# Kernel optimization log

Hardware: AMD Instinct MI355X
Metric: run time of the kernel (lower is better)

Reference implementation:

```python
import jax, jax.numpy as jnp
import numpy as np

D_MODEL = 1024
H = 16
D_K = D_MODEL // H


def setup_inputs() -> dict:
    key = jax.random.key(0)
    ks = jax.random.split(key, 11)
    B, S = 4, 2048
    scale = 1.0 / np.sqrt(D_MODEL)
    inp = {
        "q": jax.random.normal(ks[0], (B, S, D_MODEL), jnp.float32),
        "k": jax.random.normal(ks[1], (B, S, D_MODEL), jnp.float32),
        "v": jax.random.normal(ks[2], (B, S, D_MODEL), jnp.float32),
        # Linear weights stored as (in, out) so y = x @ W + b
        "W_q": jax.random.normal(ks[3], (D_MODEL, D_MODEL), jnp.float32) * scale,
        "b_q": jnp.zeros((D_MODEL,), jnp.float32),
        "W_k": jax.random.normal(ks[4], (D_MODEL, D_MODEL), jnp.float32) * scale,
        "b_k": jnp.zeros((D_MODEL,), jnp.float32),
        "W_v": jax.random.normal(ks[5], (D_MODEL, D_MODEL), jnp.float32) * scale,
        "b_v": jnp.zeros((D_MODEL,), jnp.float32),
        "W_o": jax.random.normal(ks[6], (D_MODEL, D_MODEL), jnp.float32) * scale,
        "b_o": jnp.zeros((D_MODEL,), jnp.float32),
    }
    return inp


def _split_heads(x, B):
    # (B, S, d_model) -> (B, h, S, d_k)
    return x.reshape(B, -1, H, D_K).transpose(0, 2, 1, 3)


def reference(q, k, v, W_q, b_q, W_k, b_k, W_v, b_v, W_o, b_o):
    B = q.shape[0]
    qh = _split_heads(q @ W_q + b_q, B)  # (B,h,S,dk)
    kh = _split_heads(k @ W_k + b_k, B)
    vh = _split_heads(v @ W_v + b_v, B)
    scores = jnp.einsum("bhsd,bhtd->bhst", qh, kh) / jnp.sqrt(jnp.float32(D_K))
    attn = jax.nn.softmax(scores, axis=-1)  # dropout p=0 -> identity
    out = jnp.einsum("bhst,bhtd->bhsd", attn, vh)  # (B,h,S,dk)
    out = out.transpose(0, 2, 1, 3).reshape(B, -1, H * D_K)  # merge heads
    return out @ W_o + b_o
```

## Files before the change

### kernel.cpp

```cpp
#include <hip/hip_runtime.h>

#define D_MODEL 1024
#define SEQ 2048
#define BATCH 4
#define NHEADS 16
#define HDK 64
#define MTOT (BATCH * SEQ)
#define NT (SEQ / 64)

typedef __attribute__((ext_vector_type(8))) _Float16 f16x8;
typedef __attribute__((ext_vector_type(2))) __fp16 pk16x2;
typedef __attribute__((ext_vector_type(4))) float f32x4;

__device__ inline unsigned short f2h_bits(float f) {
  _Float16 h = (_Float16)f;
  union { _Float16 h; unsigned short u; } c;
  c.h = h;
  return c.u;
}

__device__ inline unsigned pk2(float a, float b) {
  union { pk16x2 h; unsigned u; } c;
  c.h = __builtin_amdgcn_cvt_pkrtz(a, b);
  return c.u;
}

typedef __attribute__((address_space(3))) unsigned int lds_u32_t;
typedef __attribute__((address_space(1))) const unsigned int glb_u32_t;
__device__ __forceinline__ void gll16(const void* g, void* l) {
  __builtin_amdgcn_global_load_lds((glb_u32_t*)g, (lds_u32_t*)l, 16, 0, 0);
}

__global__ __launch_bounds__(256) void wtrans_kernel(
    const float* __restrict__ W0, const float* __restrict__ W1,
    const float* __restrict__ W2, const float* __restrict__ W3,
    unsigned short* __restrict__ WT) {
  __shared__ float tile[64][65];
  const float* W = blockIdx.z == 0 ? W0 : blockIdx.z == 1 ? W1
                  : blockIdx.z == 2 ? W2 : W3;
  unsigned short* out = WT + (size_t)blockIdx.z * D_MODEL * D_MODEL;
  const int k0 = blockIdx.x * 64, n0 = blockIdx.y * 64;
  const int t = threadIdx.x;
#pragma unroll
  for (int i = 0; i < 16; ++i) {
    int e = t + i * 256;
    int r = e >> 6, c = e & 63;
    tile[r][c] = W[(size_t)(k0 + r) * D_MODEL + n0 + c];
  }
  __syncthreads();
#pragma unroll
  for (int i = 0; i < 16; ++i) {
    int e = t + i * 256;
    int r = e >> 6, c = e & 63;
    int slot = (c >> 3) ^ (r & 7);
    out[(size_t)(n0 + r) * D_MODEL + k0 + slot * 8 + (c & 7)] =
        f2h_bits(tile[c][r]);
  }
}

template <bool A_F32, int OUT_MODE>
__global__ __launch_bounds__(256) void gemm_kernel(
    const void* __restrict__ Aptr, const unsigned short* __restrict__ Bt,
    const float* __restrict__ bias, void* __restrict__ Cptr) {
  __shared__ unsigned short As[128 * 64];
  __shared__ unsigned short Bs[128 * 64];
  const int t = threadIdx.x;
  const int lane = t & 63, w = t >> 6;
  const int lo16 = lane & 15, g = lane >> 4;
  const int wr = w >> 1, wc = w & 1;
  const int m0 = blockIdx.x * 128, n0 = blockIdx.y * 128;

  f32x4 acc[4][4] = {};

  const unsigned short* bgb =
      Bt + (size_t)(n0 + (t >> 3)) * D_MODEL + (t & 7) * 8;
  const float* agf = nullptr;
  const unsigned short* agh = nullptr;
  if constexpr (A_F32)
    agf = (const float*)Aptr + (size_t)(m0 + (t >> 4)) * D_MODEL + (t & 15) * 4;
  else
    agh = (const unsigned short*)Aptr + (size_t)(m0 + (t >> 3)) * D_MODEL +
          (t & 7) * 8;

  for (int kt = 0; kt < D_MODEL / 64; ++kt) {
#pragma unroll
    for (int i = 0; i < 4; ++i)
      gll16(bgb + (size_t)i * 32 * D_MODEL, &Bs[(size_t)(i * 256 + t) * 8]);
    bgb += 64;

    if constexpr (A_F32) {
#pragma unroll
      for (int i = 0; i < 8; ++i) {
        int row = (t >> 4) + i * 16, kq = (t & 15) * 4;
        float4 vv =
            *reinterpret_cast<const float4*>(agf + (size_t)i * 16 * D_MODEL);
        int slot = (kq >> 3) ^ (row & 7);
        uint2 pp;
        pp.x = pk2(vv.x, vv.y);
        pp.y = pk2(vv.z, vv.w);
        *reinterpret_cast<uint2*>(&As[row * 64 + slot * 8 + (kq & 7)]) = pp;
      }
      agf += 64;
    } else {
#pragma unroll
      for (int i = 0; i < 4; ++i)
        gll16(agh + (size_t)i * 32 * D_MODEL, &As[(size_t)(i * 256 + t) * 8]);
      agh += 64;
    }
    __syncthreads();

#pragma unroll
    for (int kk = 0; kk < 2; ++kk) {
      f16x8 af[4], bfr[4];
#pragma unroll
      for (int m = 0; m < 4; ++m) {
        int row = wr * 64 + m * 16 + lo16;
        int slot = (kk * 4 + g) ^ (row & 7);
        af[m] = *reinterpret_cast<const f16x8*>(&As[row * 64 + slot * 8]);
      }
#pragma unroll
      for (int n = 0; n < 4; ++n) {
        int row = wc * 64 + n * 16 + lo16;
        int slot = (kk * 4 + g) ^ (row & 7);
        bfr[n] = *reinterpret_cast<const f16x8*>(&Bs[row * 64 + slot * 8]);
      }
#pragma unroll
      for (int m = 0; m < 4; ++m)
#pragma unroll
        for (int n = 0; n < 4; ++n)
          acc[m][n] = __builtin_amdgcn_mfma_f32_16x16x32_f16(af[m], bfr[n],
                                                             acc[m][n], 0, 0, 0);
    }
    __syncthreads();
  }

#pragma unroll
  for (int m = 0; m < 4; ++m) {
#pragma unroll
    for (int n = 0; n < 4; ++n) {
      int col = n0 + wc * 64 + n * 16 + lo16;
      float bv = bias[col];
      if constexpr (OUT_MODE == 2) {
        int hh = col >> 6, dk = col & 63;
        int r = m0 + wr * 64 + m * 16 + g * 4;
        int bb = r >> 11, ss = r & 2047;
        ushort4 pkv;
        pkv.x = f2h_bits(acc[m][n][0] + bv);
        pkv.y = f2h_bits(acc[m][n][1] + bv);
        pkv.z = f2h_bits(acc[m][n][2] + bv);
        pkv.w = f2h_bits(acc[m][n][3] + bv);
        *reinterpret_cast<ushort4*>(
            (unsigned short*)Cptr +
            (((size_t)bb * NHEADS + hh) * HDK + dk) * SEQ + ss) = pkv;
      } else {
#pragma unroll
        for (int j = 0; j < 4; ++j) {
          int row = m0 + wr * 64 + m * 16 + g * 4 + j;
          float val = acc[m][n][j] + bv;
          if constexpr (OUT_MODE == 1) {
            ((float*)Cptr)[(size_t)row * D_MODEL + col] = val;
          } else {
            ((unsigned short*)Cptr)[(size_t)row * D_MODEL + col] = f2h_bits(val);
          }
        }
      }
    }
  }
}

__global__ __launch_bounds__(256, 3) void attn_kernel(
    const unsigned short* __restrict__ QP, const unsigned short* __restrict__ KP,
    const unsigned short* __restrict__ VPT, unsigned short* __restrict__ CTX) {
  __shared__ unsigned short Kb[2][64 * 64];
  __shared__ unsigned short Vb[2][64 * 64];
  const int t = threadIdx.x;
  const int lane = t & 63, w = t >> 6;
  const int lo16 = lane & 15, g = lane >> 4;
  const int bh = blockIdx.x & 63, qt = blockIdx.x >> 6;
  const int b = bh >> 4, h = bh & 15;
  const int q0 = qt * 128;
  const size_t rowbase = (size_t)b * SEQ;

  f16x8 qf[2][2];
#pragma unroll
  for (int nQ = 0; nQ < 2; ++nQ)
#pragma unroll
    for (int kk = 0; kk < 2; ++kk) {
      qf[nQ][kk] = *reinterpret_cast<const f16x8*>(
          QP + (rowbase + q0 + w * 32 + nQ * 16 + lo16) * D_MODEL + h * 64 +
          kk * 32 + g * 8);
      qf[nQ][kk] *= (_Float16)0.18033688f;
    }

  f32x4 o_acc[2][4] = {};
  float lsum[2] = {0.f, 0.f};

  const int r0 = t >> 3, c8i = t & 7;
  const unsigned short* kg0 =
      KP + (rowbase + r0) * D_MODEL + h * 64 + c8i * 8;
  const unsigned short* kg1 = kg0 + (size_t)32 * D_MODEL;
  const unsigned short* vg0 =
      VPT + ((size_t)bh * HDK + r0) * SEQ + c8i * 8;
  const unsigned short* vg1 = vg0 + (size_t)32 * SEQ;
  const int so0 = r0 * 64 + ((c8i ^ (r0 & 7)) * 8);
  const int so1 = (r0 + 32) * 64 + ((c8i ^ (r0 & 7)) * 8);

  {
    int4 k0v = *reinterpret_cast<const int4*>(kg0);
    int4 k1v = *reinterpret_cast<const int4*>(kg1);
    int4 v0v = *reinterpret_cast<const int4*>(vg0);
    int4 v1v = *reinterpret_cast<const int4*>(vg1);
    *reinterpret_cast<int4*>(&Kb[0][so0]) = k0v;
    *reinterpret_cast<int4*>(&Kb[0][so1]) = k1v;
    *reinterpret_cast<int4*>(&Vb[0][so0]) = v0v;
    *reinterpret_cast<int4*>(&Vb[0][so1]) = v1v;
  }
  kg0 += (size_t)64 * D_MODEL; kg1 += (size_t)64 * D_MODEL;
  vg0 += 64; vg1 += 64;
  __syncthreads();

  const bool evn = ((g & 1) == 0);
  const bool lowp = (g < 2);
  const bool isg0 = (g == 0), isg3 = (g == 3);
  int cur = 0;

  for (int kt = 0; kt < NT; ++kt) {
    int4 kreg[2], vreg[2];
    if (kt + 1 < NT) {
      kreg[0] = *reinterpret_cast<const int4*>(kg0);
      kreg[1] = *reinterpret_cast<const int4*>(kg1);
      vreg[0] = *reinterpret_cast<const int4*>(vg0);
      vreg[1] = *reinterpret_cast<const int4*>(vg1);
      kg0 += (size_t)64 * D_MODEL; kg1 += (size_t)64 * D_MODEL;
      vg0 += 64; vg1 += 64;
    }

    const unsigned short* Ksh = Kb[cur];
    const unsigned short* Vsh = Vb[cur];

    f32x4 s[4][2] = {};
#pragma unroll
    for (int kk = 0; kk < 2; ++kk) {
      f16x8 kf[4];
#pragma unroll
      for (int mK = 0; mK < 4; ++mK)
        kf[mK] = *reinterpret_cast<const f16x8*>(
            &Ksh[(mK * 16 + lo16) * 64 + (((kk * 4 + g) ^ (lo16 & 7)) * 8)]);
#pragma unroll
      for (int mK = 0; mK < 4; ++mK)
#pragma unroll
        for (int nQ = 0; nQ < 2; ++nQ)
          s[mK][nQ] = __builtin_amdgcn_mfma_f32_16x16x32_f16(
              kf[mK], qf[nQ][kk], s[mK][nQ], 0, 0, 0);
    }

#pragma unroll
    for (int nQ = 0; nQ < 2; ++nQ) {
#pragma unroll
      for (int mK = 0; mK < 4; ++mK)
#pragma unroll
        for (int j = 0; j < 4; ++j)
          s[mK][nQ][j] = __builtin_amdgcn_exp2f(s[mK][nQ][j]);
      f32x4 sm = (s[0][nQ] + s[1][nQ]) + (s[2][nQ] + s[3][nQ]);
      lsum[nQ] += (sm[0] + sm[1]) + (sm[2] + sm[3]);
    }

#pragma unroll
    for (int kk = 0; kk < 2; ++kk) {
      f16x8 pf[2];
#pragma unroll
      for (int mA = 0; mA < 2; ++mA) {
        unsigned L0 = pk2(s[2 * kk][mA][0], s[2 * kk][mA][1]);
        unsigned L1 = pk2(s[2 * kk][mA][2], s[2 * kk][mA][3]);
        unsigned H0 = pk2(s[2 * kk + 1][mA][0], s[2 * kk + 1][mA][1]);
        unsigned H1 = pk2(s[2 * kk + 1][mA][2], s[2 * kk + 1][mA][3]);
        unsigned L0x = __shfl_xor(L0, 16), L1x = __shfl_xor(L1, 16);
        unsigned H0x = __shfl_xor(H0, 16), H1x = __shfl_xor(H1, 16);
        unsigned EL0 = evn ? L0 : L0x, EL1 = evn ? L1 : L1x;
        unsigned OL0 = evn ? L0x : L0, OL1 = evn ? L1x : L1;
        unsigned EH0 = evn ? H0 : H0x, EH1 = evn ? H1 : H1x;
        unsigned OH0 = evn ? H0x : H0, OH1 = evn ? H1x : H1;
        unsigned R0 = __shfl_xor(lowp ? EH0 : EL0, 32);
        unsigned R1 = __shfl_xor(lowp ? EH1 : EL1, 32);
        unsigned R2 = __shfl_xor(lowp ? OH0 : OL0, 32);
        unsigned R3 = __shfl_xor(lowp ? OH1 : OL1, 32);
        unsigned W0 = isg0 ? EL0 : (isg3 ? EH0 : R0);
        unsigned W1 = isg0 ? EL1 : (isg3 ? EH1 : R1);
        unsigned W2 = isg0 ? OL0 : (isg3 ? OH0 : R2);
        unsigned W3 = isg0 ? OL1 : (isg3 ? OH1 : R3);
        union { uint4 u; f16x8 h; } cv;
        cv.u = make_uint4(W0, W1, W2, W3);
        pf[mA] = cv.h;
      }
      f16x8 vf[4];
#pragma unroll
      for (int n4 = 0; n4 < 4; ++n4)
        vf[n4] = *reinterpret_cast<const f16x8*>(
            &Vsh[(n4 * 16 + lo16) * 64 + (((kk * 4 + g) ^ (lo16 & 7)) * 8)]);
#pragma unroll
      for (int mA = 0; mA < 2; ++mA)
#pragma unroll
        for (int n4 = 0; n4 < 4; ++n4)
          o_acc[mA][n4] = __builtin_amdgcn_mfma_f32_16x16x32_f16(
              pf[mA], vf[n4], o_acc[mA][n4], 0, 0, 0);
    }

    if (kt + 1 < NT) {
      unsigned short* Kn = Kb[cur ^ 1];
      unsigned short* Vn = Vb[cur ^ 1];
      *reinterpret_cast<int4*>(&Kn[so0]) = kreg[0];
      *reinterpret_cast<int4*>(&Kn[so1]) = kreg[1];
      *reinterpret_cast<int4*>(&Vn[so0]) = vreg[0];
      *reinterpret_cast<int4*>(&Vn[so1]) = vreg[1];
    }
    __syncthreads();
    cur ^= 1;
  }

#pragma unroll
  for (int nQ = 0; nQ < 2; ++nQ) {
    lsum[nQ] += __shfl_xor(lsum[nQ], 16);
    lsum[nQ] += __shfl_xor(lsum[nQ], 32);
  }
  float li[2][4];
#pragma unroll
  for (int mA = 0; mA < 2; ++mA)
#pragma unroll
    for (int j = 0; j < 4; ++j)
      li[mA][j] = 1.0f / __shfl(lsum[mA], g * 4 + j);
#pragma unroll
  for (int mA = 0; mA < 2; ++mA)
#pragma unroll
    for (int n4 = 0; n4 < 4; ++n4) {
      int c8 = ((n4 * 16 + lo16) >> 3) & 7, c1 = lo16 & 7;
#pragma unroll
      for (int j = 0; j < 4; ++j) {
        size_t row = rowbase + q0 + w * 32 + mA * 16 + g * 4 + j;
        int tok7 = (g * 4 + j) & 7;
        CTX[row * D_MODEL + h * 64 + ((c8 ^ tok7) << 3) + c1] =
            f2h_bits(o_acc[mA][n4][j] * li[mA][j]);
      }
    }
}

extern "C" void kernel_launch(void* const* d_in, const int* in_sizes, int n_in,
                              void* d_out, int out_size, void* d_ws,
                              size_t ws_size, hipStream_t stream) {
  (void)in_sizes; (void)n_in; (void)out_size; (void)ws_size;
  const float* q  = (const float*)d_in[0];
  const float* k  = (const float*)d_in[1];
  const float* v  = (const float*)d_in[2];
  const float* Wq = (const float*)d_in[3];
  const float* bq = (const float*)d_in[4];
  const float* Wk = (const float*)d_in[5];
  const float* bk = (const float*)d_in[6];
  const float* Wv = (const float*)d_in[7];
  const float* bv = (const float*)d_in[8];
  const float* Wo = (const float*)d_in[9];
  const float* bo = (const float*)d_in[10];

  unsigned short* WT  = (unsigned short*)d_ws;
  unsigned short* QP  = WT + (size_t)4 * D_MODEL * D_MODEL;
  unsigned short* KP  = QP + (size_t)MTOT * D_MODEL;
  unsigned short* VPT = KP + (size_t)MTOT * D_MODEL;
  unsigned short* CTX = VPT + (size_t)MTOT * D_MODEL;

  wtrans_kernel<<<dim3(16, 16, 4), 256, 0, stream>>>(Wq, Wk, Wv, Wo, WT);

  dim3 gg(MTOT / 128, D_MODEL / 128);
  gemm_kernel<true, 0><<<gg, 256, 0, stream>>>(
      q, WT + (size_t)0 * D_MODEL * D_MODEL, bq, QP);
  gemm_kernel<true, 0><<<gg, 256, 0, stream>>>(
      k, WT + (size_t)1 * D_MODEL * D_MODEL, bk, KP);
  gemm_kernel<true, 2><<<gg, 256, 0, stream>>>(
      v, WT + (size_t)2 * D_MODEL * D_MODEL, bv, VPT);

  attn_kernel<<<1024, 256, 0, stream>>>(QP, KP, VPT, CTX);

  gemm_kernel<false, 1><<<gg, 256, 0, stream>>>(
      CTX, WT + (size_t)3 * D_MODEL * D_MODEL, bo, d_out);
}
```

Baseline: 223.8 us.

## Merge QKV projections into one launch and prefetch fp32 A tiles into registers

The three separate Q/K/V projection GEMM launches become a single launch, with blockIdx.z selecting the input, weight slice, bias and output layout. The fp32 A operand is now double-buffered in registers, so the global load for the next k-tile is issued before the current tile is converted and written to shared memory. Swizzled shared-memory offsets are precomputed once per thread. The aim is to cut launch overhead and tail effects between the projection GEMMs and to hide global load latency, at the cost of extra registers that may lower occupancy.

```diff
diff --git a/kernel.cpp b/kernel.cpp
--- a/kernel.cpp
+++ b/kernel.cpp
@@ -58,10 +58,12 @@
   }
 }
 
-template <bool A_F32, int OUT_MODE>
-__global__ __launch_bounds__(256) void gemm_kernel(
-    const void* __restrict__ Aptr, const unsigned short* __restrict__ Bt,
-    const float* __restrict__ bias, void* __restrict__ Cptr) {
+__global__ __launch_bounds__(256) void gemm_qkv_kernel(
+    const float* __restrict__ qA, const float* __restrict__ kA,
+    const float* __restrict__ vA, const unsigned short* __restrict__ WTall,
+    const float* __restrict__ bq, const float* __restrict__ bk,
+    const float* __restrict__ bv, unsigned short* __restrict__ QP,
+    unsigned short* __restrict__ KP, unsigned short* __restrict__ VPT) {
   __shared__ unsigned short As[128 * 64];
   __shared__ unsigned short Bs[128 * 64];
   const int t = threadIdx.x;
@@ -69,43 +71,43 @@
   const int lo16 = lane & 15, g = lane >> 4;
   const int wr = w >> 1, wc = w & 1;
   const int m0 = blockIdx.x * 128, n0 = blockIdx.y * 128;
+  const int z = blockIdx.z;
+  const float* Af = z == 0 ? qA : z == 1 ? kA : vA;
+  const unsigned short* Bt = WTall + (size_t)z * D_MODEL * D_MODEL;
+  const float* bias = z == 0 ? bq : z == 1 ? bk : bv;
 
   f32x4 acc[4][4] = {};
 
   const unsigned short* bgb =
       Bt + (size_t)(n0 + (t >> 3)) * D_MODEL + (t & 7) * 8;
-  const float* agf = nullptr;
-  const unsigned short* agh = nullptr;
-  if constexpr (A_F32)
-    agf = (const float*)Aptr + (size_t)(m0 + (t >> 4)) * D_MODEL + (t & 15) * 4;
-  else
-    agh = (const unsigned short*)Aptr + (size_t)(m0 + (t >> 3)) * D_MODEL +
-          (t & 7) * 8;
-
-  for (int kt = 0; kt < D_MODEL / 64; ++kt) {
+  const int arow = t >> 4, akq = (t & 15) * 4;
+  const float* agf = Af + (size_t)(m0 + arow) * D_MODEL + akq;
+  int aso[8];
+#pragma unroll
+  for (int i = 0; i < 8; ++i) {
+    int row = arow + i * 16;
+    aso[i] = row * 64 + (((akq >> 3) ^ (row & 7)) * 8) + (akq & 7);
+  }
+
+  auto LOADA = [&](float4 (&ar)[8], int kt) {
+    const float* p = agf + kt * 64;
+#pragma unroll
+    for (int i = 0; i < 8; ++i)
+      ar[i] = *reinterpret_cast<const float4*>(p + (size_t)i * 16 * D_MODEL);
+  };
+
+  auto BODY = [&](int kt, float4 (&cura)[8], float4 (&nxta)[8]) {
 #pragma unroll
     for (int i = 0; i < 4; ++i)
-      gll16(bgb + (size_t)i * 32 * D_MODEL, &Bs[(size_t)(i * 256 + t) * 8]);
-    bgb += 64;
-
-    if constexpr (A_F32) {
-#pragma unroll
-      for (int i = 0; i < 8; ++i) {
-        int row = (t >> 4) + i * 16, kq = (t & 15) * 4;
-        float4 vv =
-            *reinterpret_cast<const float4*>(agf + (size_t)i * 16 * D_MODEL);
-        int slot = (kq >> 3) ^ (row & 7);
-        uint2 pp;
-        pp.x = pk2(vv.x, vv.y);
-        pp.y = pk2(vv.z, vv.w);
-        *reinterpret_cast<uint2*>(&As[row * 64 + slot * 8 + (kq & 7)]) = pp;
-      }
-      agf += 64;
-    } else {
-#pragma unroll
-      for (int i = 0; i < 4; ++i)
-        gll16(agh + (size_t)i * 32 * D_MODEL, &As[(size_t)(i * 256 + t) * 8]);
-      agh += 64;
+      gll16(bgb + (size_t)i * 32 * D_MODEL + kt * 64,
+            &Bs[(size_t)(i * 256 + t) * 8]);
+    if (kt + 1 < D_MODEL / 64) LOADA(nxta, kt + 1);
+#pragma unroll
+    for (int i = 0; i < 8; ++i) {
+      uint2 pp;
+      pp.x = pk2(cura[i].x, cura[i].y);
+      pp.y = pk2(cura[i].z, cura[i].w);
+      *reinterpret_cast<uint2*>(&As[aso[i]]) = pp;
     }
     __syncthreads();
 
@@ -132,6 +134,14 @@
                                                              acc[m][n], 0, 0, 0);
     }
     __syncthreads();
+  };
+
+  float4 arA[8], arB[8];
+  LOADA(arA, 0);
+#pragma unroll
+  for (int kt = 0; kt < D_MODEL / 64; kt += 2) {
+    BODY(kt, arA, arB);
+    BODY(kt + 1, arB, arA);
   }
 
 #pragma unroll
@@ -139,30 +149,94 @@
 #pragma unroll
     for (int n = 0; n < 4; ++n) {
       int col = n0 + wc * 64 + n * 16 + lo16;
-      float bv = bias[col];
-      if constexpr (OUT_MODE == 2) {
+      float bvv = bias[col];
+      if (z == 2) {
         int hh = col >> 6, dk = col & 63;
         int r = m0 + wr * 64 + m * 16 + g * 4;
         int bb = r >> 11, ss = r & 2047;
         ushort4 pkv;
-        pkv.x = f2h_bits(acc[m][n][0] + bv);
-        pkv.y = f2h_bits(acc[m][n][1] + bv);
-        pkv.z = f2h_bits(acc[m][n][2] + bv);
-        pkv.w = f2h_bits(acc[m][n][3] + bv);
+        pkv.x = f2h_bits(acc[m][n][0] + bvv);
+        pkv.y = f2h_bits(acc[m][n][1] + bvv);
+        pkv.z = f2h_bits(acc[m][n][2] + bvv);
+        pkv.w = f2h_bits(acc[m][n][3] + bvv);
         *reinterpret_cast<ushort4*>(
-            (unsigned short*)Cptr +
-            (((size_t)bb * NHEADS + hh) * HDK + dk) * SEQ + ss) = pkv;
+            VPT + (((size_t)bb * NHEADS + hh) * HDK + dk) * SEQ + ss) = pkv;
       } else {
+        unsigned short* outp = (z == 0) ? QP : KP;
 #pragma unroll
         for (int j = 0; j < 4; ++j) {
           int row = m0 + wr * 64 + m * 16 + g * 4 + j;
-          float val = acc[m][n][j] + bv;
-          if constexpr (OUT_MODE == 1) {
-            ((float*)Cptr)[(size_t)row * D_MODEL + col] = val;
-          } else {
-            ((unsigned short*)Cptr)[(size_t)row * D_MODEL + col] = f2h_bits(val);
-          }
+          outp[(size_t)row * D_MODEL + col] = f2h_bits(acc[m][n][j] + bvv);
         }
+      }
+    }
+  }
+}
+
+__global__ __launch_bounds__(256) void gemm_o_kernel(
+    const unsigned short* __restrict__ Actx, const unsigned short* __restrict__ Bt,
+    const float* __restrict__ bias, float* __restrict__ Cptr) {
+  __shared__ unsigned short As[128 * 64];
+  __shared__ unsigned short Bs[128 * 64];
+  const int t = threadIdx.x;
+  const int lane = t & 63, w = t >> 6;
+  const int lo16 = lane & 15, g = lane >> 4;
+  const int wr = w >> 1, wc = w & 1;
+  const int m0 = blockIdx.x * 128, n0 = blockIdx.y * 128;
+
+  f32x4 acc[4][4] = {};
+
+  const unsigned short* bgb =
+      Bt + (size_t)(n0 + (t >> 3)) * D_MODEL + (t & 7) * 8;
+  const unsigned short* agh =
+      Actx + (size_t)(m0 + (t >> 3)) * D_MODEL + (t & 7) * 8;
+
+  for (int kt = 0; kt < D_MODEL / 64; ++kt) {
+#pragma unroll
+    for (int i = 0; i < 4; ++i)
+      gll16(bgb + (size_t)i * 32 * D_MODEL, &Bs[(size_t)(i * 256 + t) * 8]);
+    bgb += 64;
+#pragma unroll
+    for (int i = 0; i < 4; ++i)
+      gll16(agh + (size_t)i * 32 * D_MODEL, &As[(size_t)(i * 256 + t) * 8]);
+    agh += 64;
+    __syncthreads();
+
+#pragma unroll
+    for (int kk = 0; kk < 2; ++kk) {
+      f16x8 af[4], bfr[4];
+#pragma unroll
+      for (int m = 0; m < 4; ++m) {
+        int row = wr * 64 + m * 16 + lo16;
+        int slot = (kk * 4 + g) ^ (row & 7);
+        af[m] = *reinterpret_cast<const f16x8*>(&As[row * 64 + slot * 8]);
+      }
+#pragma unroll
+      for (int n = 0; n < 4; ++n) {
+        int row = wc * 64 + n * 16 + lo16;
+        int slot = (kk * 4 + g) ^ (row & 7);
+        bfr[n] = *reinterpret_cast<const f16x8*>(&Bs[row * 64 + slot * 8]);
+      }
+#pragma unroll
+      for (int m = 0; m < 4; ++m)
+#pragma unroll
+        for (int n = 0; n < 4; ++n)
+          acc[m][n] = __builtin_amdgcn_mfma_f32_16x16x32_f16(af[m], bfr[n],
+                                                             acc[m][n], 0, 0, 0);
+    }
+    __syncthreads();
+  }
+
+#pragma unroll
+  for (int m = 0; m < 4; ++m) {
+#pragma unroll
+    for (int n = 0; n < 4; ++n) {
+      int col = n0 + wc * 64 + n * 16 + lo16;
+      float bv = bias[col];
+#pragma unroll
+      for (int j = 0; j < 4; ++j) {
+        int row = m0 + wr * 64 + m * 16 + g * 4 + j;
+        Cptr[(size_t)row * D_MODEL + col] = acc[m][n][j] + bv;
       }
     }
   }
@@ -367,16 +441,11 @@
 
   wtrans_kernel<<<dim3(16, 16, 4), 256, 0, stream>>>(Wq, Wk, Wv, Wo, WT);
 
-  dim3 gg(MTOT / 128, D_MODEL / 128);
-  gemm_kernel<true, 0><<<gg, 256, 0, stream>>>(
-      q, WT + (size_t)0 * D_MODEL * D_MODEL, bq, QP);
-  gemm_kernel<true, 0><<<gg, 256, 0, stream>>>(
-      k, WT + (size_t)1 * D_MODEL * D_MODEL, bk, KP);
-  gemm_kernel<true, 2><<<gg, 256, 0, stream>>>(
-      v, WT + (size_t)2 * D_MODEL * D_MODEL, bv, VPT);
+  gemm_qkv_kernel<<<dim3(MTOT / 128, D_MODEL / 128, 3), 256, 0, stream>>>(
+      q, k, v, WT, bq, bk, bv, QP, KP, VPT);
 
   attn_kernel<<<1024, 256, 0, stream>>>(QP, KP, VPT, CTX);
 
-  gemm_kernel<false, 1><<<gg, 256, 0, stream>>>(
-      CTX, WT + (size_t)3 * D_MODEL * D_MODEL, bo, d_out);
-}
+  gemm_o_kernel<<<dim3(MTOT / 128, D_MODEL / 128), 256, 0, stream>>>(
+      CTX, WT + (size_t)3 * D_MODEL * D_MODEL, bo, (float*)d_out);
+}
```

New measurement: 207.5 us, median of 2. 1.08x faster.
